# Kernel tuning notes

Measured on AMD Instinct MI355X. Metric: run time of the kernel, lower is better.

The kernel has to match this reference:

```python
import jax, jax.numpy as jnp
import numpy as np

# CSC-FC connectivity constants (match init_kwargs)
C = 8192   # input features (csc_c)
N = 8192   # output features (csc_n)
F = 64     # fan-in per output neuron (csc_f)
S = 1      # stride of connectivity window (csc_s)
B = 128    # batch

# Precompute gather indices: output neuron j connects to inputs (j*S + k) % C, k in [0, F)
_IDX = (np.arange(N, dtype=np.int32)[:, None] * S + np.arange(F, dtype=np.int32)[None, :]) % C  # [N, F]


def setup_inputs() -> dict:
    key = jax.random.key(0)
    k1, k2 = jax.random.split(key)
    x = jax.random.normal(k1, (B, C), dtype=jnp.float32)
    kernel = jax.random.normal(k2, (C, N), dtype=jnp.float32) * 0.05
    bias = jnp.zeros((N,), dtype=jnp.float32)
    return {"x": x, "kernel": kernel, "bias": bias}


def reference(x, kernel, bias):
    idx = jnp.asarray(_IDX)                      # [N, F] int32
    cols = jnp.arange(N, dtype=jnp.int32)[:, None]
    w_g = kernel[idx, cols]                      # [N, F] gathered sparse weights
    x_g = x[:, idx]                              # [B, N, F] gathered inputs
    # out[b, n] = sum_f x_g[b, n, f] * w_g[n, f] + bias[n]
    return jnp.einsum('bnf,nf->bn', x_g, w_g) + bias
```

## Files before the change

### kernel.cpp

```cpp
#include <hip/hip_runtime.h>

#define C_DIM 8192
#define N_DIM 8192
#define B_DIM 128
#define TN 128
#define TB 16
#define XW 196
#define WS 132
#define NROWS (TN + 63)

typedef float f4 __attribute__((ext_vector_type(4)));

__global__ __launch_bounds__(256) void cscfc_kernel(
    const float* __restrict__ x,
    const float* __restrict__ K,
    const float* __restrict__ bias,
    float* __restrict__ out)
{
    __shared__ float x_s[TB * XW];
    __shared__ float w_t[64 * WS];

    const int t    = threadIdx.x;
    const int lane = t & 63;
    const int rg   = t >> 6;
    const int n0   = blockIdx.x * TN;
    const int b0   = blockIdx.y * TB;

    #pragma unroll
    for (int pass = 0; pass < 4; ++pass) {
        const int b_loc = pass * 4 + rg;
        const float* __restrict__ xr = x + (size_t)(b0 + b_loc) * C_DIM;
        #pragma unroll
        for (int k = 0; k < 3; ++k) {
            const int cc = lane + 64 * k;
            x_s[b_loc * XW + cc] = xr[(n0 + cc) & (C_DIM - 1)];
        }
    }

    for (int p = 0; p < 48; ++p) {
        const int rr = p * 4 + rg;
        if (rr < NROWS) {
            const int nlo   = (rr - 63 > 0) ? rr - 63 : 0;
            const int nhi   = (rr < TN - 1) ? rr : TN - 1;
            const int n_loc = nlo + lane;
            if (n_loc <= nhi) {
                const int c = (n0 + rr) & (C_DIM - 1);
                const int f = rr - n_loc;
                w_t[f * WS + n_loc] = K[(size_t)c * N_DIM + (n0 + n_loc)];
            }
        }
    }
    __syncthreads();

    const int ng     = lane & 31;
    const int n_base = ng * 4;
    const int bg     = (lane >> 5) | (rg << 1);
    const int bl0    = bg;
    const int bl1    = bg + 8;

    float acc0[4] = {0.f, 0.f, 0.f, 0.f};
    float acc1[4] = {0.f, 0.f, 0.f, 0.f};

    #pragma unroll 4
    for (int f0 = 0; f0 < 64; f0 += 4) {
        const f4 w0 = *(const f4*)&w_t[(f0 + 0) * WS + n_base];
        const f4 w1 = *(const f4*)&w_t[(f0 + 1) * WS + n_base];
        const f4 w2 = *(const f4*)&w_t[(f0 + 2) * WS + n_base];
        const f4 w3 = *(const f4*)&w_t[(f0 + 3) * WS + n_base];

        const float* xs0 = &x_s[bl0 * XW + n_base + f0];
        const f4 xa = *(const f4*)(xs0);
        const f4 xb = *(const f4*)(xs0 + 4);
        acc0[0] = fmaf(xa.x, w0.x, fmaf(xa.y, w1.x, fmaf(xa.z, w2.x, fmaf(xa.w, w3.x, acc0[0]))));
        acc0[1] = fmaf(xa.y, w0.y, fmaf(xa.z, w1.y, fmaf(xa.w, w2.y, fmaf(xb.x, w3.y, acc0[1]))));
        acc0[2] = fmaf(xa.z, w0.z, fmaf(xa.w, w1.z, fmaf(xb.x, w2.z, fmaf(xb.y, w3.z, acc0[2]))));
        acc0[3] = fmaf(xa.w, w0.w, fmaf(xb.x, w1.w, fmaf(xb.y, w2.w, fmaf(xb.z, w3.w, acc0[3]))));

        const float* xs1 = &x_s[bl1 * XW + n_base + f0];
        const f4 xc = *(const f4*)(xs1);
        const f4 xd = *(const f4*)(xs1 + 4);
        acc1[0] = fmaf(xc.x, w0.x, fmaf(xc.y, w1.x, fmaf(xc.z, w2.x, fmaf(xc.w, w3.x, acc1[0]))));
        acc1[1] = fmaf(xc.y, w0.y, fmaf(xc.z, w1.y, fmaf(xc.w, w2.y, fmaf(xd.x, w3.y, acc1[1]))));
        acc1[2] = fmaf(xc.z, w0.z, fmaf(xc.w, w1.z, fmaf(xd.x, w2.z, fmaf(xd.y, w3.z, acc1[2]))));
        acc1[3] = fmaf(xc.w, w0.w, fmaf(xd.x, w1.w, fmaf(xd.y, w2.w, fmaf(xd.z, w3.w, acc1[3]))));
    }

    const f4 bv = *(const f4*)(bias + n0 + n_base);
    f4 o0, o1;
    o0.x = acc0[0] + bv.x; o0.y = acc0[1] + bv.y; o0.z = acc0[2] + bv.z; o0.w = acc0[3] + bv.w;
    o1.x = acc1[0] + bv.x; o1.y = acc1[1] + bv.y; o1.z = acc1[2] + bv.z; o1.w = acc1[3] + bv.w;
    *(f4*)(out + (size_t)(b0 + bl0) * N_DIM + n0 + n_base) = o0;
    *(f4*)(out + (size_t)(b0 + bl1) * N_DIM + n0 + n_base) = o1;
}

extern "C" void kernel_launch(void* const* d_in, const int* in_sizes, int n_in,
                              void* d_out, int out_size, void* d_ws, size_t ws_size,
                              hipStream_t stream) {
    const float* x    = (const float*)d_in[0];
    const float* K    = (const float*)d_in[1];
    const float* bias = (const float*)d_in[2];
    float* out = (float*)d_out;

    dim3 grid(N_DIM / TN, B_DIM / TB, 1);
    dim3 block(256, 1, 1);
    cscfc_kernel<<<grid, block, 0, stream>>>(x, K, bias, out);
}
```

Baseline: 321.0 us.

## Vectorize x and K band loads into registers before scattering to LDS

Replaces the scalar per-row global loads of x and the diagonal K band with float4 loads issued up front into registers (16 K vectors and 4 x vectors per thread), then scatters them into shared memory with a bounds test. The band is covered by rectangular 4-wide chunks, so some loaded elements outside the diagonal band are discarded, and the x tile is widened to 256 columns. The goal is fewer, wider, coalesced global transactions with all loads in flight at once instead of 48 dependent scalar load passes. It costs extra register pressure and some redundant bandwidth.

```diff
diff --git a/kernel.cpp b/kernel.cpp
--- a/kernel.cpp
+++ b/kernel.cpp
@@ -5,9 +5,8 @@
 #define B_DIM 128
 #define TN 128
 #define TB 16
-#define XW 196
+#define XW 260
 #define WS 132
-#define NROWS (TN + 63)
 
 typedef float f4 __attribute__((ext_vector_type(4)));
 
@@ -26,28 +25,44 @@
     const int n0   = blockIdx.x * TN;
     const int b0   = blockIdx.y * TB;
 
+    f4 xq[4];
     #pragma unroll
-    for (int pass = 0; pass < 4; ++pass) {
-        const int b_loc = pass * 4 + rg;
-        const float* __restrict__ xr = x + (size_t)(b0 + b_loc) * C_DIM;
-        #pragma unroll
-        for (int k = 0; k < 3; ++k) {
-            const int cc = lane + 64 * k;
-            x_s[b_loc * XW + cc] = xr[(n0 + cc) & (C_DIM - 1)];
-        }
+    for (int i = 0; i < 4; ++i) {
+        const int g   = t + 256 * i;
+        const int row = g >> 6;
+        const int col = (g & 63) * 4;
+        xq[i] = *(const f4*)&x[(size_t)(b0 + row) * C_DIM + ((n0 + col) & (C_DIM - 1))];
     }
 
-    for (int p = 0; p < 48; ++p) {
-        const int rr = p * 4 + rg;
-        if (rr < NROWS) {
-            const int nlo   = (rr - 63 > 0) ? rr - 63 : 0;
-            const int nhi   = (rr < TN - 1) ? rr : TN - 1;
-            const int n_loc = nlo + lane;
-            if (n_loc <= nhi) {
-                const int c = (n0 + rr) & (C_DIM - 1);
-                const int f = rr - n_loc;
-                w_t[f * WS + n_loc] = K[(size_t)c * N_DIM + (n0 + n_loc)];
-            }
+    f4 kq[16];
+    int krow[16], kcol[16];
+    #pragma unroll
+    for (int i = 0; i < 16; ++i) {
+        const int g = t + 256 * i;
+        int rr, qc;
+        if (g < 1024)      { rr = g >> 4;                    qc = g & 15; }
+        else if (g < 3072) { const int h = g - 1024; rr = 64 + (h >> 5); qc = h & 31; }
+        else               { const int h = g - 3072; rr = 128 + (h >> 4); qc = 16 + (h & 15); }
+        krow[i] = rr;
+        kcol[i] = qc * 4;
+        const int c = (n0 + rr) & (C_DIM - 1);
+        kq[i] = *(const f4*)&K[(size_t)c * N_DIM + n0 + qc * 4];
+    }
+
+    #pragma unroll
+    for (int i = 0; i < 4; ++i) {
+        const int g   = t + 256 * i;
+        const int row = g >> 6;
+        const int col = (g & 63) * 4;
+        *(f4*)&x_s[row * XW + col] = xq[i];
+    }
+    #pragma unroll
+    for (int i = 0; i < 16; ++i) {
+        #pragma unroll
+        for (int k = 0; k < 4; ++k) {
+            const int n_loc = kcol[i] + k;
+            const int f     = krow[i] - n_loc;
+            if ((unsigned)f < 64u) w_t[f * WS + n_loc] = kq[i][k];
         }
     }
     __syncthreads();
```

New measurement: 301.0 us. 6.2% less time.
